# Performance work log

Hardware: AMD Instinct MI355X
Metric: run time of the kernel (lower is better)

The kernel has to match this reference:

```python
import jax, jax.numpy as jnp
import numpy as np
import math

LAYERS = 30
LAYERS_PER_STACK = 10  # layers // stacks
SCALES = [4, 4, 4, 4]  # total upsampling 256
SQRT_HALF = math.sqrt(0.5)


def _dilated_conv1d(x, w, b, dilation):
    # x: (B, Cin, T), w: (Cout, Cin, K), non-causal SAME padding
    p = (w.shape[-1] - 1) // 2 * dilation
    y = jax.lax.conv_general_dilated(
        x, w, window_strides=(1,), padding=[(p, p)],
        rhs_dilation=(dilation,), dimension_numbers=('NCH', 'OIH', 'NCH'))
    return y + b[None, :, None]


def _conv1x1(x, w):
    # x: (B, Cin, T), w: (Cout, Cin)
    return jnp.einsum('oc,bct->bot', w, x)


def _upsample(c, W_cin, W_up):
    # ConvInUpsampleNetwork with aux_context_window=0: 1x1 conv_in (no bias)
    c = _conv1x1(c, W_cin)                      # (B, 80, T')
    u = c[:, None]                              # (B, 1, 80, T')
    for i, s in enumerate(SCALES):
        u = jnp.repeat(u, s, axis=-1)           # Stretch2d nearest along time
        u = jax.lax.conv_general_dilated(
            u, W_up[i], window_strides=(1, 1), padding=[(0, 0), (s, s)],
            dimension_numbers=('NCHW', 'OIHW', 'NCHW'))  # kernel (1, 2s+1), no bias
    return u[:, 0]                              # (B, 80, T)


def setup_inputs() -> dict:
    key = jax.random.key(0)
    ks = jax.random.split(key, 20)
    B, T_frames, T = 2, 128, 32768
    rc, gc, sc, ac = 64, 128, 64, 80
    sd = 0.05
    inp = {
        'x': jax.random.normal(ks[0], (B, 1, T), jnp.float32),
        'c': jax.random.normal(ks[1], (B, ac, T_frames), jnp.float32),
        'W_first': jax.random.normal(ks[2], (rc, 1), jnp.float32) * sd,
        'b_first': jnp.zeros((rc,), jnp.float32),
        'W_cin': jax.random.normal(ks[3], (ac, ac), jnp.float32) * sd,
        'W_up': jax.random.normal(ks[4], (len(SCALES), 1, 1, 1, 9), jnp.float32) * 0.1
                + 1.0 / 9.0,  # near averaging-filter init
        'Wd': jax.random.normal(ks[5], (LAYERS, gc, rc, 3), jnp.float32) * sd,
        'bd': jnp.zeros((LAYERS, gc), jnp.float32),
        'Wa': jax.random.normal(ks[6], (LAYERS, gc, ac), jnp.float32) * sd,
        'Ws': jax.random.normal(ks[7], (LAYERS, sc, gc // 2), jnp.float32) * sd,
        'bs': jnp.zeros((LAYERS, sc), jnp.float32),
        'Wr': jax.random.normal(ks[8], (LAYERS, rc, gc // 2), jnp.float32) * sd,
        'br': jnp.zeros((LAYERS, rc), jnp.float32),
        'Wl1': jax.random.normal(ks[9], (sc, sc), jnp.float32) * sd,
        'bl1': jnp.zeros((sc,), jnp.float32),
        'Wl2': jax.random.normal(ks[10], (1, sc), jnp.float32) * sd,
        'bl2': jnp.zeros((1,), jnp.float32),
    }
    return inp


def reference(x, c, W_first, b_first, W_cin, W_up, Wd, bd, Wa, Ws, bs, Wr, br,
              Wl1, bl1, Wl2, bl2):
    # upsample conditioning to sample rate
    c_up = _upsample(c, W_cin, W_up)            # (B, 80, T)
    # first 1x1 conv
    h = _conv1x1(x, W_first) + b_first[None, :, None]  # (B, 64, T)
    skips = jnp.zeros_like(_conv1x1(h, Ws[0]))  # (B, 64, T) placeholder shape
    skips = 0.0
    for i in range(LAYERS):
        d = 2 ** (i % LAYERS_PER_STACK)
        g = _dilated_conv1d(h, Wd[i], bd[i], d)            # (B, 128, T)
        g = g + _conv1x1(c_up, Wa[i])                      # aux conditioning
        xa, xb = jnp.split(g, 2, axis=1)
        z = jnp.tanh(xa) * jax.nn.sigmoid(xb)              # (B, 64, T)
        skips = skips + _conv1x1(z, Ws[i]) + bs[i][None, :, None]
        h = (_conv1x1(z, Wr[i]) + br[i][None, :, None] + h) * SQRT_HALF
    skips = skips * math.sqrt(1.0 / LAYERS)
    y = jax.nn.relu(skips)
    y = _conv1x1(y, Wl1) + bl1[None, :, None]
    y = jax.nn.relu(y)
    y = _conv1x1(y, Wl2) + bl2[None, :, None]
    return y  # (B, 1, T)
```

## Files before the change

kernel.cpp:

```cpp
#include <hip/hip_runtime.h>
#include <math.h>

#define T_LEN 32768
#define NLAYERS 30
#define NBLK 512
#define SQRT_HALF 0.70710678118654752f
#define C30 0.18257418583505537f

typedef short short8 __attribute__((ext_vector_type(8)));
typedef short short4v __attribute__((ext_vector_type(4)));
typedef float float4v __attribute__((ext_vector_type(4)));
typedef unsigned short u16;
typedef unsigned long long u64t;
typedef u64t u64x2 __attribute__((ext_vector_type(2)));

__device__ inline u16 rne_bf16(float f){
    unsigned u = __builtin_bit_cast(unsigned, f);
    u += 0x7fffu + ((u >> 16) & 1u);
    return (u16)(u >> 16);
}
__device__ inline float bf16_to_f32(u16 h){
    unsigned u = ((unsigned)h) << 16;
    return __builtin_bit_cast(float, u);
}

__device__ inline u64t ld_sys(const u16* p){
    return __hip_atomic_load((const u64t*)p, __ATOMIC_RELAXED, __HIP_MEMORY_SCOPE_SYSTEM);
}
__device__ inline void st_sys(u16* p, u64t v){
    __hip_atomic_store((u64t*)p, v, __ATOMIC_RELAXED, __HIP_MEMORY_SCOPE_SYSTEM);
}
__device__ inline unsigned ld_sys32(const unsigned* p){
    return __hip_atomic_load(p, __ATOMIC_RELAXED, __HIP_MEMORY_SCOPE_SYSTEM);
}
__device__ inline void st_sys32(unsigned* p, unsigned v){
    __hip_atomic_store(p, v, __ATOMIC_RELAXED, __HIP_MEMORY_SCOPE_SYSTEM);
}
__device__ inline unsigned ld_ag(const unsigned* p){
    return __hip_atomic_load(p, __ATOMIC_RELAXED, __HIP_MEMORY_SCOPE_AGENT);
}
__device__ inline void st_ag(unsigned* p, unsigned v){
    __hip_atomic_store(p, v, __ATOMIC_RELAXED, __HIP_MEMORY_SCOPE_AGENT);
}

__global__ void prep_wmain(const float* __restrict__ Wd, const float* __restrict__ Wa,
                           u16* __restrict__ WA)
{
    int idx = blockIdx.x * 256 + threadIdx.x;
    if (idx >= NLAYERS * 9 * 8 * 64) return;
    int lane = idx & 63;
    int mb = (idx >> 6) & 7;
    int cc = (idx >> 9) % 9;
    int l_ = (idx >> 9) / 9;
    int m = mb * 16 + (lane & 15);
    int kbase = cc * 32 + (lane >> 4) * 8;
    size_t base = ((size_t)(l_ * 9 + cc)) * 4096 + mb * 512 + lane * 8;
#pragma unroll
    for (int j = 0; j < 8; ++j) {
        int k = kbase + j;
        float v = 0.f;
        if (k < 192) {
            int tap = k >> 6, i = k & 63;
            v = Wd[((size_t)(l_ * 128 + m) * 64 + i) * 3 + tap];
        } else if (k < 272) {
            v = Wa[(size_t)(l_ * 128 + m) * 80 + (k - 192)];
        }
        WA[base + j] = rne_bf16(v);
    }
}

__global__ void prep_wsr(const float* __restrict__ Ws, const float* __restrict__ Wr,
                         u16* __restrict__ W2)
{
    int idx = blockIdx.x * 256 + threadIdx.x;
    if (idx >= NLAYERS * 2 * 8 * 64) return;
    int lane = idx & 63;
    int mb = (idx >> 6) & 7;
    int cc = (idx >> 9) & 1;
    int l_ = idx >> 10;
    int m2 = mb * 16 + (lane & 15);
    int kbase = cc * 32 + (lane >> 4) * 8;
    size_t base = ((size_t)(l_ * 2 + cc)) * 4096 + mb * 512 + lane * 8;
#pragma unroll
    for (int j = 0; j < 8; ++j) {
        int k2 = kbase + j;
        float v = (m2 < 64) ? Ws[(size_t)(l_ * 64 + m2) * 64 + k2]
                            : Wr[(size_t)(l_ * 64 + (m2 - 64)) * 64 + k2];
        W2[base + j] = rne_bf16(v);
    }
}

__global__ void cin_kernel(const float* __restrict__ c, const float* __restrict__ Wcin,
                           float* __restrict__ c1)
{
    int idx = blockIdx.x * 256 + threadIdx.x;
    if (idx >= 2 * 128 * 80) return;
    int o = idx % 80;
    int f = (idx / 80) & 127;
    int b = idx / (80 * 128);
    float acc = 0.f;
    for (int ch = 0; ch < 80; ++ch)
        acc = fmaf(Wcin[o * 80 + ch], c[(b * 80 + ch) * 128 + f], acc);
    c1[idx] = acc;
}

__global__ void up_kernel(const float* __restrict__ in, float* __restrict__ out,
                          const float* __restrict__ w9, int Win)
{
    int idx = blockIdx.x * 256 + threadIdx.x;
    int Wout = Win * 4;
    int total = 2 * Wout * 80;
    if (idx >= total) return;
    int a = idx % 80;
    int t = (idx / 80) % Wout;
    int b = idx / (80 * Wout);
    const float* ip = in + (size_t)b * Win * 80 + a;
    float acc = 0.f;
#pragma unroll
    for (int j = 0; j < 9; ++j) {
        int q = t + j - 4;
        if (q >= 0 && q < Wout) acc = fmaf(w9[j], ip[(size_t)(q >> 2) * 80], acc);
    }
    out[idx] = acc;
}

__global__ void upfinal_kernel(const float* __restrict__ u3, const float* __restrict__ w9,
                               u16* __restrict__ cup)
{
    int idx = blockIdx.x * 256 + threadIdx.x;
    if (idx >= 2 * T_LEN * 96) return;
    int a = idx % 96;
    int t = (idx / 96) & (T_LEN - 1);
    int b = idx / (96 * T_LEN);
    float acc = 0.f;
    if (a < 80) {
        const float* ip = u3 + (size_t)b * 8192 * 80 + a;
#pragma unroll
        for (int j = 0; j < 9; ++j) {
            int q = t + j - 4;
            if (q >= 0 && q < T_LEN) acc = fmaf(w9[j], ip[(size_t)(q >> 2) * 80], acc);
        }
    }
    cup[idx] = rne_bf16(acc);
}

__global__ void bar_init(unsigned* bar){
    int i = blockIdx.x * 256 + threadIdx.x;
    for (int e = i; e < 33792; e += 256 * 64) bar[e] = 0u;
}

__global__ __launch_bounds__(512, 4) void wavenet_kernel(
    const float* __restrict__ x, const float* __restrict__ Wf, const float* __restrict__ bf,
    u16* __restrict__ h0, u16* __restrict__ h1,
    u16* __restrict__ m0, u16* __restrict__ m1,
    const u16* __restrict__ cup,
    const u16* __restrict__ WA_all, const u16* __restrict__ W2_all,
    const float* __restrict__ bd_all, const float* __restrict__ bs_all,
    const float* __restrict__ br_all,
    const float* __restrict__ Wl1, const float* __restrict__ bl1,
    const float* __restrict__ Wl2, const float* __restrict__ bl2,
    float* __restrict__ y, unsigned* __restrict__ bar, unsigned* __restrict__ xcdmap)
{
    __shared__ u16 wa_sm[36864];
    const int tid = threadIdx.x;
    const int l  = tid & 63;
    const int w  = tid >> 6;
    const int lr = l & 15;
    const int lg = l >> 4;
    const int bx = blockIdx.x;
    const int g  = ((bx & 7) << 6) | (bx >> 3);
    const int b  = g >> 8;
    const int gt = g & 255;
    const int t0blk = gt * 128;
    const int n0 = t0blk + w * 16;
    char* zb = (char*)wa_sm + w * 4096;

    unsigned* flagP = bar + 1024;

    int dil_cur = 1;
    long toff[3];
    unsigned tmir = 0;

    auto grid_bar = [&](int k){
        __syncthreads();
        if (tid == 0) {
            const unsigned epoch = (unsigned)(k + 1);
            const int grp = bx & 7;
            unsigned* arr  = bar + grp * 32;
            unsigned* root = bar + 8 * 32;
            unsigned* rel  = bar + 9 * 32 + grp * 32;
            unsigned old = __hip_atomic_fetch_add(arr, 1u, __ATOMIC_RELAXED, __HIP_MEMORY_SCOPE_AGENT);
            if (old == epoch * 64u - 1u) {
                unsigned ro = __hip_atomic_fetch_add(root, 1u, __ATOMIC_RELAXED, __HIP_MEMORY_SCOPE_AGENT);
                if (ro == epoch * 8u - 1u) {
#pragma unroll
                    for (int j = 0; j < 8; ++j)
                        __hip_atomic_store(bar + 9 * 32 + j * 32, epoch, __ATOMIC_RELAXED, __HIP_MEMORY_SCOPE_AGENT);
                }
            }
            while (__hip_atomic_load(rel, __ATOMIC_RELAXED, __HIP_MEMORY_SCOPE_AGENT) < epoch)
                __builtin_amdgcn_s_sleep(16);
        }
        __syncthreads();
        asm volatile("buffer_inv" ::: "memory");
    };

    auto wait_nb = [&](const unsigned* fl, unsigned tgt){
        if (tid < 9 && tid != 4) {
            int jt = gt - 4 + tid;
            if (jt >= 0 && jt < 256) {
                const unsigned* fp = fl + (size_t)(b * 256 + jt) * 32;
                while (ld_ag(fp) < tgt) __builtin_amdgcn_s_sleep(4);
            }
        }
        __syncthreads();
    };

    auto wld = [&](const u16* Wg, int c){ return *(const short8*)(Wg + (size_t)c * 4096 + tid * 8); };
    auto wst = [&](int c, short8 v){ *(short8*)((char*)wa_sm + c * 8192 + tid * 16) = v; };

    unsigned myxcd;
    asm volatile("s_getreg_b32 %0, hwreg(HW_REG_XCC_ID)" : "=s"(myxcd));
    if (tid == 0) st_sys32(xcdmap + g, myxcd);
    grid_bar(0);

    unsigned fmask = 0;
    for (int i = 0; i < 11; ++i) {
        int j = gt - 5 + i;
        if (i != 5 && j >= 0 && j < 256) {
            unsigned xv = ld_sys32(xcdmap + b * 256 + j);
            if (xv != myxcd) fmask |= 1u << i;
        }
    }
    int lkT = -1000000, rkT = 1000000;
    for (int i = 4; i >= 0; --i) if ((fmask >> i) & 1) { lkT = t0blk + 128 * (i - 4) - 1; break; }
    for (int i = 6; i <= 10; ++i) if ((fmask >> i) & 1) { rkT = t0blk + 128 * (i - 5); break; }

    u16* hih = h0;
    u16* hoh = h1;
    u16* mih = m0;
    u16* moh = m1;
    const short8 zero8 = (short8)0;

    auto prep_taps = [&](){
        tmir = 0;
#pragma unroll
        for (int tap = 0; tap < 3; ++tap) {
            int offd = (tap - 1) * dil_cur;
            toff[tap] = ((long)b * T_LEN + n0 + offd) * 64;
            int ws0 = n0 + offd;
            int a0 = ws0 < 0 ? 0 : ws0;
            int a1 = (ws0 + 15 >= T_LEN) ? (T_LEN - 1) : (ws0 + 15);
            if (a0 <= a1) {
                int i_0 = (a0 >> 7) - gt + 5;
                int i_1 = (a1 >> 7) - gt + 5;
                if (((fmask >> i_0) & 1) || ((fmask >> i_1) & 1)) tmir |= 1u << tap;
            }
        }
    };

    auto issue_bfrag = [&](int cc, short8& BH){
        if (cc < 6) {
            const int tap = cc >> 1;
            const int i0 = (cc & 1) * 32 + lg * 8;
            int t = n0 + lr + (tap - 1) * dil_cur;
            if ((unsigned)t < (unsigned)T_LEN) {
                long off = toff[tap] + lr * 64 + i0;
                if ((tmir >> tap) & 1) {
                    u64x2 qh;
                    qh.x = ld_sys(mih + off); qh.y = ld_sys(mih + off + 4);
                    BH = __builtin_bit_cast(short8, qh);
                } else {
                    BH = *(const short8*)(hih + off);
                }
            } else { BH = zero8; }
        } else {
            const int a0 = (cc - 6) * 32 + lg * 8;
            int t = n0 + lr;
            BH = *(const short8*)(cup + ((size_t)b * T_LEN + t) * 96 + a0);
        }
    };

#pragma unroll
    for (int e = 0; e < 4; ++e) {
        int q = e * 512 + tid;
        int tl = q >> 4, ch0 = (q & 15) * 4;
        int t = t0blk + tl;
        size_t bt = (size_t)b * T_LEN + t;
        float xv = x[bt];
        short4v hv4;
#pragma unroll
        for (int r = 0; r < 4; ++r) {
            float v = fmaf(Wf[ch0 + r], xv, bf[ch0 + r]);
            hv4[r] = (short)rne_bf16(v);
        }
        *(short4v*)(h0 + bt * 64 + ch0) = hv4;
        if ((t - lkT <= 33) || (rkT - t <= 33))
            st_sys(m0 + bt * 64 + ch0, __builtin_bit_cast(u64t, hv4));
    }

    float4v skipacc[4];
#pragma unroll
    for (int mb = 0; mb < 4; ++mb) skipacc[mb] = (float4v)0.f;

    __syncthreads();
    if (tid == 0) st_ag(flagP + (size_t)g * 32, 1u);

    {
        short8 r0 = wld(WA_all, 0), r1 = wld(WA_all, 1), r2 = wld(WA_all, 2), r3 = wld(WA_all, 3);
        short8 r4 = wld(WA_all, 4), r5 = wld(WA_all, 5), r6 = wld(WA_all, 6),
               r7 = wld(WA_all, 7), r8 = wld(WA_all, 8);
        wst(0, r0); wst(1, r1); wst(2, r2); wst(3, r3);
        wst(4, r4); wst(5, r5); wst(6, r6); wst(7, r7); wst(8, r8);
        __syncthreads();
    }

    for (int l_ = 0; l_ < NLAYERS; ++l_) {
        dil_cur = 1 << (l_ % 10);
        const int dnext = (l_ < NLAYERS - 1) ? (1 << ((l_ + 1) % 10)) : 0;
        const int thr = dnext + 32;
        const u16* WAn = WA_all + (size_t)(l_ + 1) * 9 * 4096;
        const u16* W2 = W2_all + (size_t)l_ * 2 * 4096;
        const float* bd = bd_all + l_ * 128;
        const float* bs = bs_all + l_ * 64;
        const float* br = br_all + l_ * 64;

        prep_taps();
        wait_nb(flagP, (unsigned)(l_ + 1));
        asm volatile("buffer_inv" ::: "memory");

        float4v acc[8];
#pragma unroll
        for (int mb = 0; mb < 8; ++mb) acc[mb] = (float4v)0.f;

        short8 p0, p1, p2;
        issue_bfrag(0, p0);
        issue_bfrag(1, p1);
        issue_bfrag(2, p2);
#pragma unroll
        for (int cc = 0; cc < 9; ++cc) {
            short8 bh;
            if ((cc % 3) == 0)      { bh = p0; if (cc + 3 < 9) issue_bfrag(cc + 3, p0); }
            else if ((cc % 3) == 1) { bh = p1; if (cc + 3 < 9) issue_bfrag(cc + 3, p1); }
            else                    { bh = p2; if (cc + 3 < 9) issue_bfrag(cc + 3, p2); }
            const char* cbuf = (const char*)wa_sm + cc * 8192;
#pragma unroll
            for (int mb = 0; mb < 8; ++mb) {
                short8 ah = *(const short8*)(cbuf + mb * 1024 + l * 16);
                acc[mb] = __builtin_amdgcn_mfma_f32_16x16x32_bf16(ah, bh, acc[mb], 0, 0, 0);
            }
        }
        __syncthreads();

        short4v ehq[4];
        {
            int t = n0 + lr;
#pragma unroll
            for (int m = 0; m < 4; ++m) {
                size_t off = ((size_t)b * T_LEN + t) * 64 + m * 16 + lg * 4;
                ehq[m] = *(const short4v*)(hih + off);
            }
        }

#pragma unroll
        for (int mb = 0; mb < 4; ++mb) {
            const float4v bda = *(const float4v*)(bd + mb * 16 + lg * 4);
            const float4v bdb = *(const float4v*)(bd + 64 + mb * 16 + lg * 4);
            int t = lr;
            short4v zhv;
#pragma unroll
            for (int r = 0; r < 4; ++r) {
                float xa = acc[mb][r] + bda[r];
                float xb = acc[mb + 4][r] + bdb[r];
                float e2 = __expf(2.f * xa);
                float e3 = __expf(-xb);
                float tnum = e2 - 1.f;
                float tden = e2 + 1.f;
                float den = fmaf(tden, e3, tden);
                float z = tnum * __builtin_amdgcn_rcpf(den);
                zhv[r] = (short)rne_bf16(z);
            }
            unsigned byteoff = (unsigned)((t * 64 + mb * 16 + lg * 4) * 2) ^ ((unsigned)(t & 7) << 4);
            *(short4v*)(zb + byteoff) = zhv;
        }

        if (l_ != NLAYERS - 1) {
            short8 r4 = wld(WAn, 4), r5 = wld(WAn, 5), r6 = wld(WAn, 6),
                   r7 = wld(WAn, 7), r8 = wld(WAn, 8);
            wst(4, r4); wst(5, r5); wst(6, r6); wst(7, r7); wst(8, r8);
        }

        float4v acc2[8];
#pragma unroll
        for (int mb = 0; mb < 8; ++mb) acc2[mb] = (float4v)0.f;

#pragma unroll
        for (int c2 = 0; c2 < 2; ++c2) {
            int t = lr;
            unsigned k0 = (unsigned)(c2 * 32 + lg * 8);
            unsigned byteoff = (unsigned)((t * 64 + k0) * 2) ^ ((unsigned)(t & 7) << 4);
            short8 b2h = *(const short8*)(zb + byteoff);
#pragma unroll
            for (int mb = 0; mb < 8; ++mb) {
                short8 ah = *(const short8*)(W2 + (size_t)c2 * 4096 + mb * 512 + l * 8);
                acc2[mb] = __builtin_amdgcn_mfma_f32_16x16x32_bf16(ah, b2h, acc2[mb], 0, 0, 0);
            }
        }

#pragma unroll
        for (int mb = 0; mb < 8; ++mb) {
            int ch0 = (mb & 3) * 16 + lg * 4;
            if (mb < 4) {
                const float4v bsv = *(const float4v*)(bs + ch0);
                skipacc[mb] = skipacc[mb] + acc2[mb] + bsv;
            } else if (l_ != NLAYERS - 1) {
                const float4v brv = *(const float4v*)(br + ch0);
                int t = n0 + lr;
                size_t off = ((size_t)b * T_LEN + t) * 64 + ch0;
                short4v hv = ehq[mb - 4];
                short4v ohv;
#pragma unroll
                for (int r = 0; r < 4; ++r) {
                    float hr = bf16_to_f32((u16)hv[r]);
                    float xo = (acc2[mb][r] + brv[r] + hr) * SQRT_HALF;
                    ohv[r] = (short)rne_bf16(xo);
                }
                *(short4v*)(hoh + off) = ohv;
                if ((t - lkT <= thr) || (rkT - t <= thr))
                    st_sys(moh + off, __builtin_bit_cast(u64t, ohv));
            }
        }

        if (l_ != NLAYERS - 1) {
            __syncthreads();
            if (tid == 0) st_ag(flagP + (size_t)g * 32, (unsigned)(l_ + 2));
            short8 r0 = wld(WAn, 0), r1 = wld(WAn, 1), r2 = wld(WAn, 2), r3 = wld(WAn, 3);
            wst(0, r0); wst(1, r1); wst(2, r2); wst(3, r3);
            __syncthreads();
        }
        u16* t1;
        t1 = hih; hih = hoh; hoh = t1;
        t1 = mih; mih = moh; moh = t1;
    }

    __syncthreads();
    char* sk = (char*)wa_sm;
#pragma unroll
    for (int mb = 0; mb < 4; ++mb) {
        int tloc = w * 16 + lr;
        int ch0 = mb * 16 + lg * 4;
        unsigned off = (unsigned)((tloc * 64 + ch0) * 4) ^ ((unsigned)(tloc & 7) << 5);
        *(float4v*)(sk + off) = skipacc[mb];
    }
    float* w1s = (float*)((char*)wa_sm + 32768);
    for (int e = tid; e < 4096; e += 512) w1s[e] = Wl1[e];
    __syncthreads();
    if (tid < 128) {
        int tloc = tid;
        float s[64];
#pragma unroll
        for (int i4 = 0; i4 < 16; ++i4) {
            unsigned off = (unsigned)((tloc * 64 + i4 * 4) * 4) ^ ((unsigned)(tloc & 7) << 5);
            float4v v = *(const float4v*)(sk + off);
#pragma unroll
            for (int r = 0; r < 4; ++r) s[i4 * 4 + r] = fmaxf(v[r] * C30, 0.f);
        }
        float acc = bl2[0];
        for (int o = 0; o < 64; ++o) {
            float a = bl1[o];
#pragma unroll
            for (int i = 0; i < 64; ++i) a = fmaf(w1s[o * 64 + i], s[i], a);
            acc = fmaf(Wl2[o], fmaxf(a, 0.f), acc);
        }
        y[(size_t)b * T_LEN + t0blk + tloc] = acc;
    }
}

extern "C" void kernel_launch(void* const* d_in, const int* in_sizes, int n_in,
                              void* d_out, int out_size, void* d_ws, size_t ws_size,
                              hipStream_t stream)
{
    const float* x       = (const float*)d_in[0];
    const float* c       = (const float*)d_in[1];
    const float* W_first = (const float*)d_in[2];
    const float* b_first = (const float*)d_in[3];
    const float* W_cin   = (const float*)d_in[4];
    const float* W_up    = (const float*)d_in[5];
    const float* Wd      = (const float*)d_in[6];
    const float* bd      = (const float*)d_in[7];
    const float* Wa      = (const float*)d_in[8];
    const float* Ws      = (const float*)d_in[9];
    const float* bs      = (const float*)d_in[10];
    const float* Wr      = (const float*)d_in[11];
    const float* br      = (const float*)d_in[12];
    const float* Wl1     = (const float*)d_in[13];
    const float* bl1     = (const float*)d_in[14];
    const float* Wl2     = (const float*)d_in[15];
    const float* bl2     = (const float*)d_in[16];

    char* base = (char*)d_ws;
    size_t off = 0;
    auto alloc = [&](size_t bytes) { char* p = base + off; off += (bytes + 255) & ~(size_t)255; return p; };

    const size_t HSZ = (size_t)2 * T_LEN * 64 * 2;
    u16* cup  = (u16*)alloc((size_t)2 * T_LEN * 96 * 2);
    u16* h0   = (u16*)alloc(HSZ);
    u16* h1   = (u16*)alloc(HSZ);
    u16* m0   = (u16*)alloc(HSZ);
    u16* m1   = (u16*)alloc(HSZ);
    unsigned* bar    = (unsigned*)alloc(33792 * 4);
    unsigned* xcdmap = (unsigned*)alloc(4096);
    char* S = alloc(7200000);
    float* c1 = (float*)(S);
    float* u1 = (float*)(S + 81920);
    float* u2 = (float*)(S + 409600);
    float* u3 = (float*)(S + 1720320);
    u16* WA = (u16*)(S);
    u16* W2 = (u16*)(S + 2211840);

    cin_kernel<<<(2 * 128 * 80 + 255) / 256, 256, 0, stream>>>(c, W_cin, c1);
    up_kernel<<<(2 * 512 * 80 + 255) / 256, 256, 0, stream>>>(c1, u1, W_up + 0, 128);
    up_kernel<<<(2 * 2048 * 80 + 255) / 256, 256, 0, stream>>>(u1, u2, W_up + 9, 512);
    up_kernel<<<(2 * 8192 * 80 + 255) / 256, 256, 0, stream>>>(u2, u3, W_up + 18, 2048);
    upfinal_kernel<<<(2 * T_LEN * 96 + 255) / 256, 256, 0, stream>>>(u3, W_up + 27, cup);

    prep_wmain<<<(NLAYERS * 9 * 8 * 64 + 255) / 256, 256, 0, stream>>>(Wd, Wa, WA);
    prep_wsr<<<(NLAYERS * 2 * 8 * 64 + 255) / 256, 256, 0, stream>>>(Ws, Wr, W2);
    bar_init<<<64, 256, 0, stream>>>(bar);

    wavenet_kernel<<<NBLK, 512, 0, stream>>>(
        x, W_first, b_first,
        h0, h1, m0, m1,
        cup, WA, W2,
        bd, bs, br, Wl1, bl1, Wl2, bl2,
        (float*)d_out, bar, xcdmap);
}
```

Baseline: 526.1 us.

## Compute local chunks before waiting on neighbor flags, shorten spin sleep

Splits the nine K-chunks of the dilated-conv MFMA loop so the chunks that depend only on locally owned data (2,3,6,7,8) run before the neighbor-readiness wait. The chunks that need neighbor tiles (0,1,4,5) run after the wait and cache invalidate. This overlaps inter-block synchronization latency with useful compute. The spin-wait sleep is also shortened to poll flags more often. Risk: correctness relies on chunks 2,3,6,7,8 truly not touching neighbor-written data, and the three-deep prefetch ring is replaced by batch issue with more live registers.

```diff
diff --git a/kernel.cpp b/kernel.cpp
--- a/kernel.cpp
+++ b/kernel.cpp
@@ -210,7 +210,7 @@
             int jt = gt - 4 + tid;
             if (jt >= 0 && jt < 256) {
                 const unsigned* fp = fl + (size_t)(b * 256 + jt) * 32;
-                while (ld_ag(fp) < tgt) __builtin_amdgcn_s_sleep(4);
+                while (ld_ag(fp) < tgt) __builtin_amdgcn_s_sleep(1);
             }
         }
         __syncthreads();
@@ -326,29 +326,47 @@
         const float* br = br_all + l_ * 64;
 
         prep_taps();
-        wait_nb(flagP, (unsigned)(l_ + 1));
-        asm volatile("buffer_inv" ::: "memory");
 
         float4v acc[8];
 #pragma unroll
         for (int mb = 0; mb < 8; ++mb) acc[mb] = (float4v)0.f;
 
-        short8 p0, p1, p2;
-        issue_bfrag(0, p0);
-        issue_bfrag(1, p1);
-        issue_bfrag(2, p2);
-#pragma unroll
-        for (int cc = 0; cc < 9; ++cc) {
-            short8 bh;
-            if ((cc % 3) == 0)      { bh = p0; if (cc + 3 < 9) issue_bfrag(cc + 3, p0); }
-            else if ((cc % 3) == 1) { bh = p1; if (cc + 3 < 9) issue_bfrag(cc + 3, p1); }
-            else                    { bh = p2; if (cc + 3 < 9) issue_bfrag(cc + 3, p2); }
+        auto do_chunk = [&](int cc, short8 bh){
             const char* cbuf = (const char*)wa_sm + cc * 8192;
 #pragma unroll
             for (int mb = 0; mb < 8; ++mb) {
                 short8 ah = *(const short8*)(cbuf + mb * 1024 + l * 16);
                 acc[mb] = __builtin_amdgcn_mfma_f32_16x16x32_bf16(ah, bh, acc[mb], 0, 0, 0);
             }
+        };
+
+        {
+            short8 a2, a3, a6, a7, a8;
+            issue_bfrag(2, a2);
+            issue_bfrag(3, a3);
+            issue_bfrag(6, a6);
+            issue_bfrag(7, a7);
+            issue_bfrag(8, a8);
+            do_chunk(2, a2);
+            do_chunk(3, a3);
+            do_chunk(6, a6);
+            do_chunk(7, a7);
+            do_chunk(8, a8);
+        }
+
+        wait_nb(flagP, (unsigned)(l_ + 1));
+        asm volatile("buffer_inv" ::: "memory");
+
+        {
+            short8 b0, b1, b4, b5;
+            issue_bfrag(0, b0);
+            issue_bfrag(1, b1);
+            issue_bfrag(4, b4);
+            issue_bfrag(5, b5);
+            do_chunk(0, b0);
+            do_chunk(1, b1);
+            do_chunk(4, b4);
+            do_chunk(5, b5);
         }
         __syncthreads();
 
```

After: 540.8 us. 2.8% more time.
